# Kernel optimization log

Hardware: AMD Instinct MI355X
Metric: run time of the kernel (lower is better)

Reference implementation:

```python
import jax, jax.numpy as jnp
import numpy as np

N0, E0 = 50000, 200000
N1 = E0 // 2          # 100000 path nodes (pairs of graph0 edges)
E1 = 400000
ATOM_F, BOND_F, IN_F, H = 128, 128, 64, 2


def _egat(src, dst, n_nodes, nfeats, efeats, W_ni, W_nj, W_fij, W_node, b_node, attn, bias, out_n, out_e):
    # edge feature: f_ni[src] + f_nj[dst] + fc_fij(efeats) + bias
    f = (nfeats @ W_ni)[src] + (nfeats @ W_nj)[dst] + efeats @ W_fij + bias
    f = jax.nn.leaky_relu(f).reshape(-1, H, out_e)          # [E, H, out_e]
    e = jnp.sum(f * attn, axis=-1)                          # [E, H] attention logits
    # edge softmax over incoming edges of each dst node
    emax = jax.ops.segment_max(e, dst, num_segments=n_nodes)
    ee = jnp.exp(e - emax[dst])
    a = ee / jax.ops.segment_sum(ee, dst, num_segments=n_nodes)[dst]   # [E, H]
    h = (nfeats @ W_node + b_node).reshape(-1, H, out_n)    # [N, H, out_n]
    h_out = jax.ops.segment_sum(h[src] * a[..., None], dst, num_segments=n_nodes)
    return h_out, f


def setup_inputs() -> dict:
    key = jax.random.key(0)
    it = iter(jax.random.split(key, 64))
    def nrm(shape, s=0.1):
        return jax.random.normal(next(it), shape, jnp.float32) * s
    inp = {
        'node_feats': nrm((N0, ATOM_F), 1.0),
        'edge_feats': nrm((E0, BOND_F), 1.0),
        'node_path': nrm((N1, BOND_F), 1.0),
        'edge_path': nrm((E1, IN_F), 1.0),
    }
    def egat_params(pre, in_n, in_e, out_n, out_e):
        inp[pre + '_ni'] = nrm((in_n, out_e * H))
        inp[pre + '_nj'] = nrm((in_n, out_e * H))
        inp[pre + '_fij'] = nrm((in_e, out_e * H))
        inp[pre + '_node'] = nrm((in_n, out_n * H))
        inp[pre + '_bnode'] = nrm((out_n * H,))
        inp[pre + '_attn'] = nrm((1, H, out_e))
        inp[pre + '_bias'] = nrm((out_e * H,))
    egat_params('L1', ATOM_F, BOND_F, ATOM_F, BOND_F)
    egat_params('L2a', BOND_F, IN_F, BOND_F, IN_F)
    egat_params('L2b', BOND_F, IN_F, BOND_F, IN_F)
    egat_params('L3', ATOM_F, BOND_F, ATOM_F, BOND_F)
    inp['lin1_W'] = nrm((2 * BOND_F, BOND_F))
    inp['lin1_b'] = nrm((BOND_F,))
    # graphs: arange prefix on dst guarantees in-degree >= 1 for every node
    inp['src0'] = jax.random.randint(next(it), (E0,), 0, N0)
    inp['dst0'] = jnp.concatenate([jnp.arange(N0), jax.random.randint(next(it), (E0 - N0,), 0, N0)])
    inp['src1'] = jax.random.randint(next(it), (E1,), 0, N1)
    inp['dst1'] = jnp.concatenate([jnp.arange(N1), jax.random.randint(next(it), (E1 - N1,), 0, N1)])
    return inp


def reference(node_feats, edge_feats, node_path, edge_path,
              L1_ni, L1_nj, L1_fij, L1_node, L1_bnode, L1_attn, L1_bias,
              L2a_ni, L2a_nj, L2a_fij, L2a_node, L2a_bnode, L2a_attn, L2a_bias,
              L2b_ni, L2b_nj, L2b_fij, L2b_node, L2b_bnode, L2b_attn, L2b_bias,
              L3_ni, L3_nj, L3_fij, L3_node, L3_bnode, L3_attn, L3_bias,
              lin1_W, lin1_b, src0, dst0, src1, dst1):
    ini_y3 = node_path
    # ---- stage 1: EGAT on atom graph ----
    h, f = _egat(src0, dst0, N0, node_feats, edge_feats,
                 L1_ni, L1_nj, L1_fij, L1_node, L1_bnode, L1_attn, L1_bias, ATOM_F, BOND_F)
    nf = h.sum(axis=1)            # [N0, ATOM_F]
    ef = f.sum(axis=1)            # [E0, BOND_F]
    # ---- edge-pair -> path-node lift ----
    x11 = jnp.concatenate([ef[0::2], ef[1::2]], axis=1)     # [N1, 2*BOND_F]
    node_path = x11 @ lin1_W + lin1_b + ini_y3              # [N1, BOND_F]
    # ---- stage 2: EGAT layers on path graph ----
    for p in ((L2a_ni, L2a_nj, L2a_fij, L2a_node, L2a_bnode, L2a_attn, L2a_bias),
              (L2b_ni, L2b_nj, L2b_fij, L2b_node, L2b_bnode, L2b_attn, L2b_bias)):
        h, f = _egat(src1, dst1, N1, node_path, edge_path, *p, BOND_F, IN_F)
        node_path = h.sum(axis=1)  # [N1, BOND_F]
        edge_path = f.sum(axis=1)  # [E1, IN_F]
    # ---- path-node -> edge feats for atom graph (each row repeated twice) ----
    ef2 = jnp.repeat(node_path, 2, axis=0)                  # [E0, BOND_F]
    # ---- stage 3: EGAT on atom graph again ----
    h, f = _egat(src0, dst0, N0, nf, ef2,
                 L3_ni, L3_nj, L3_fij, L3_node, L3_bnode, L3_attn, L3_bias, ATOM_F, BOND_F)
    nf = h.sum(axis=1)
    ef2 = f.sum(axis=1)
    return (nf, ef2, node_path, edge_path)
```

## Files before the change

### kernel.cpp

```cpp
#include <hip/hip_runtime.h>

#define CN0 50000
#define CE0 200000
#define CN1 100000
#define CE1 400000

typedef __attribute__((ext_vector_type(8))) _Float16 half8;
typedef __attribute__((ext_vector_type(4))) _Float16 half4;
typedef __attribute__((ext_vector_type(4))) float floatx4;

__global__ void fill_k(float* __restrict__ p, float v, int n) {
    int i = blockIdx.x * 256 + threadIdx.x;
    if (i < n) p[i] = v;
}

struct WtDesc { const float* W; _Float16* T; int KM; int mshift; int K; };
struct WtArgs { WtDesc d[17]; };

__global__ __launch_bounds__(256) void wcvt_k(WtArgs a) {
    WtDesc w = a.d[blockIdx.y];
    const int M1 = (1 << w.mshift) - 1;
    for (int i = blockIdx.x * 256 + threadIdx.x; i < w.KM; i += 256 * gridDim.x) {
        int k = i >> w.mshift, m = i & M1;
        w.T[(long)m * w.K + k] = (_Float16)w.W[i];
    }
}

__global__ void hist2_k(const int* __restrict__ dst0, const int* __restrict__ dst1,
                        int* __restrict__ deg0, int* __restrict__ deg1) {
    int i = blockIdx.x * 256 + threadIdx.x;
    if (i < CE0) atomicAdd(&deg0[dst0[i]], 1);
    if (i < CE1) atomicAdd(&deg1[dst1[i]], 1);
}

__global__ __launch_bounds__(256) void scanA_k(const int* __restrict__ deg, int N,
                                               int* __restrict__ off, int* __restrict__ bsum) {
    __shared__ int s[256];
    int t = threadIdx.x, i = blockIdx.x * 256 + t;
    int v = (i < N) ? deg[i] : 0;
    s[t] = v; __syncthreads();
    #pragma unroll
    for (int d = 1; d < 256; d <<= 1) {
        int x = (t >= d) ? s[t - d] : 0;
        __syncthreads(); s[t] += x; __syncthreads();
    }
    if (i < N) off[i] = s[t] - v;
    if (t == 255) bsum[blockIdx.x] = s[255];
}

__global__ __launch_bounds__(256) void scanB_k(int* __restrict__ bsum0, int nb0,
                                               int* __restrict__ bsum1, int nb1) {
    int* bs = blockIdx.x ? bsum1 : bsum0;
    int nb  = blockIdx.x ? nb1 : nb0;
    __shared__ int s[256];
    __shared__ int tot, carry;
    int t = threadIdx.x;
    if (t == 0) carry = 0;
    __syncthreads();
    for (int base = 0; base < nb; base += 256) {
        int i = base + t;
        int v = (i < nb) ? bs[i] : 0;
        s[t] = v; __syncthreads();
        #pragma unroll
        for (int d = 1; d < 256; d <<= 1) {
            int x = (t >= d) ? s[t - d] : 0;
            __syncthreads(); s[t] += x; __syncthreads();
        }
        if (i < nb) bs[i] = s[t] - v + carry;
        if (t == 255) tot = s[255];
        __syncthreads();
        if (t == 0) carry += tot;
        __syncthreads();
    }
}

__global__ void scanC_k(int* __restrict__ off, const int* __restrict__ bsum, int N, int E) {
    int i = blockIdx.x * 256 + threadIdx.x;
    if (i < N) off[i] += bsum[i >> 8];
    if (i == 0) off[N] = E;
}

__global__ void csrfill2_k(const int* __restrict__ dst0, const int* __restrict__ off0,
                           int* __restrict__ cur0, int* __restrict__ eidx0,
                           const int* __restrict__ dst1, const int* __restrict__ off1,
                           int* __restrict__ cur1, int* __restrict__ eidx1) {
    int i = blockIdx.x * 256 + threadIdx.x;
    if (i < CE0) {
        int d = dst0[i];
        int s = atomicAdd(&cur0[d], 1);
        eidx0[off0[d] + s] = i;
    }
    if (i < CE1) {
        int d = dst1[i];
        int s = atomicAdd(&cur1[d], 1);
        eidx1[off1[d] + s] = i;
    }
}

__global__ __launch_bounds__(256) void gemm_k(
        const float* __restrict__ X, const _Float16* __restrict__ Wt,
        const float* __restrict__ bias, const float* __restrict__ add,
        float* __restrict__ Y, int N, int K, int M) {
    __shared__ _Float16 As[128 * 64];
    char* asb = (char*)As;
    const int tid = threadIdx.x;
    const int lane = tid & 63;
    const int wid = tid >> 6;
    const int wr = wid >> 1, wc = wid & 1;
    const int bm = blockIdx.y * 128;
    const int bn = blockIdx.x * 128;
    const int l15 = lane & 15, lk = lane >> 4;

    floatx4 acc[4][4] = {};

    for (int k0 = 0; k0 < K; k0 += 64) {
        #pragma unroll
        for (int i = 0; i < 8; ++i) {
            int f = tid + i * 256;
            int r = f >> 4, kq = f & 15;
            int gr = bm + r;
            float4 v = make_float4(0.f, 0.f, 0.f, 0.f);
            if (gr < N) v = *(const float4*)&X[(long)gr * K + k0 + kq * 4];
            half4 hv = { (_Float16)v.x, (_Float16)v.y, (_Float16)v.z, (_Float16)v.w };
            int byte = (r * 128 + kq * 8) ^ ((r & 7) << 4);
            *(half4*)(asb + byte) = hv;
        }
        half8 bf[2][4];
        #pragma unroll
        for (int kk = 0; kk < 2; ++kk)
            #pragma unroll
            for (int ct = 0; ct < 4; ++ct) {
                int col = bn + wc * 64 + ct * 16 + l15;
                bf[kk][ct] = *(const half8*)&Wt[(long)col * K + k0 + kk * 32 + lk * 8];
            }
        __syncthreads();
        #pragma unroll
        for (int kk = 0; kk < 2; ++kk) {
            half8 af[4];
            #pragma unroll
            for (int rt = 0; rt < 4; ++rt) {
                int row = wr * 64 + rt * 16 + l15;
                int byte = (row * 128 + (kk * 32 + lk * 8) * 2) ^ ((row & 7) << 4);
                af[rt] = *(const half8*)(asb + byte);
            }
            #pragma unroll
            for (int rt = 0; rt < 4; ++rt)
                #pragma unroll
                for (int ct = 0; ct < 4; ++ct)
                    acc[rt][ct] = __builtin_amdgcn_mfma_f32_16x16x32_f16(
                        af[rt], bf[kk][ct], acc[rt][ct], 0, 0, 0);
        }
        __syncthreads();
    }
    #pragma unroll
    for (int ct = 0; ct < 4; ++ct) {
        int col = bn + wc * 64 + ct * 16 + l15;
        float bv = bias ? bias[col] : 0.f;
        #pragma unroll
        for (int rt = 0; rt < 4; ++rt) {
            #pragma unroll
            for (int r = 0; r < 4; ++r) {
                int row = bm + wr * 64 + rt * 16 + lk * 4 + r;
                if (row < N) {
                    float v = acc[rt][ct][r] + bv;
                    long off = (long)row * M + col;
                    if (add) v += add[off];
                    Y[off] = v;
                }
            }
        }
    }
}

__global__ __launch_bounds__(256) void edge_k(
        const float* __restrict__ FNi, const float* __restrict__ FNj,
        const float* __restrict__ FEb, const float* __restrict__ attn,
        const int* __restrict__ src, const int* __restrict__ dst,
        int E, int out_e, int fe_shift,
        float* __restrict__ ef_out, float* __restrict__ logits) {
    int e = blockIdx.x * 4 + (threadIdx.x >> 6);
    int lane = threadIdx.x & 63;
    if (e >= E) return;
    int s = src[e], d = dst[e];
    long fi = (long)s * (2 * out_e);
    long fj = (long)d * (2 * out_e);
    long fe = (long)(e >> fe_shift) * (2 * out_e);
    float l0 = 0.f, l1 = 0.f;
    for (int c = lane; c < out_e; c += 64) {
        float f0 = FNi[fi + c] + FNj[fj + c] + FEb[fe + c];
        f0 = f0 > 0.f ? f0 : 0.01f * f0;
        float f1 = FNi[fi + out_e + c] + FNj[fj + out_e + c] + FEb[fe + out_e + c];
        f1 = f1 > 0.f ? f1 : 0.01f * f1;
        l0 += f0 * attn[c];
        l1 += f1 * attn[out_e + c];
        ef_out[(long)e * out_e + c] = f0 + f1;
    }
    #pragma unroll
    for (int off = 32; off > 0; off >>= 1) {
        l0 += __shfl_down(l0, off);
        l1 += __shfl_down(l1, off);
    }
    if (lane == 0) { logits[2 * e] = l0; logits[2 * e + 1] = l1; }
}

__global__ __launch_bounds__(256) void aggregate_k(
        const float* __restrict__ Hn, const float* __restrict__ logits,
        const int* __restrict__ off, const int* __restrict__ eidx,
        const int* __restrict__ src, int N, float* __restrict__ out) {
    int n = blockIdx.x * 4 + (threadIdx.x >> 6);
    int lane = threadIdx.x & 63;
    if (n >= N) return;
    int i0 = off[n], i1 = off[n + 1];
    float m0 = -3.0e38f, m1 = -3.0e38f;
    for (int i = i0; i < i1; ++i) {
        int e = eidx[i];
        m0 = fmaxf(m0, logits[2 * e]);
        m1 = fmaxf(m1, logits[2 * e + 1]);
    }
    float s0 = 0.f, s1 = 0.f;
    for (int i = i0; i < i1; ++i) {
        int e = eidx[i];
        s0 += __expf(logits[2 * e]     - m0);
        s1 += __expf(logits[2 * e + 1] - m1);
    }
    float r0 = 1.f / s0, r1 = 1.f / s1;
    float acc0 = 0.f, acc1 = 0.f;
    for (int i = i0; i < i1; ++i) {
        int e = eidx[i];
        float w0 = __expf(logits[2 * e]     - m0) * r0;
        float w1 = __expf(logits[2 * e + 1] - m1) * r1;
        const float* h = Hn + (long)src[e] * 256;
        acc0 += w0 * h[lane]      + w1 * h[128 + lane];
        acc1 += w0 * h[64 + lane] + w1 * h[192 + lane];
    }
    float* o = out + (long)n * 128;
    o[lane]      = acc0;
    o[64 + lane] = acc1;
}

extern "C" void kernel_launch(void* const* d_in, const int* in_sizes, int n_in,
                              void* d_out, int out_size, void* d_ws, size_t ws_size,
                              hipStream_t stream) {
    const float* node_feats   = (const float*)d_in[0];
    const float* edge_feats   = (const float*)d_in[1];
    const float* node_path_in = (const float*)d_in[2];
    const float* edge_path_in = (const float*)d_in[3];
    const float* lin1_b = (const float*)d_in[33];
    const int* src0 = (const int*)d_in[34];
    const int* dst0 = (const int*)d_in[35];
    const int* src1 = (const int*)d_in[36];
    const int* dst1 = (const int*)d_in[37];

    float* out  = (float*)d_out;
    float* seg0 = out;
    float* seg1 = out + 6400000;
    float* seg2 = out + 32000000;
    float* seg3 = out + 44800000;

    float* ws     = (float*)d_ws;
    float* FNi    = ws;
    float* FNj    = FNi + 12800000;
    float* Hn     = FNj + 12800000;
    float* FE     = Hn  + 25600000;
    float* EF     = FE  + 51200000;
    float* np2    = EF  + 25600000;
    float* logits = np2 + 12800000;
    _Float16* WT  = (_Float16*)(logits + 800000);
    int* ib    = (int*)(WT + 442368);
    int* off0  = ib;
    int* eidx0 = off0 + 50001;
    int* off1  = eidx0 + 200000;
    int* eidx1 = off1 + 100001;
    int* deg0  = eidx1 + 400000;
    int* cur0  = deg0 + 50000;
    int* deg1  = cur0 + 50000;
    int* cur1  = deg1 + 100000;
    int* bsum0 = cur1 + 100000;
    int* bsum1 = bsum0 + 196;

    const int nb0 = (CN0 + 255) / 256;
    const int nb1 = (CN1 + 255) / 256;

    static const int wi_din[17]  = {4,5,6,7, 11,12,13,14, 18,19,20,21, 25,26,27,28, 32};
    static const int wi_K[17]    = {128,128,128,128, 128,128,64,128, 128,128,64,128, 128,128,128,128, 256};
    static const int wi_M[17]    = {256,256,256,256, 128,128,128,256, 128,128,128,256, 256,256,256,256, 128};
    _Float16* wt[17];
    {
        _Float16* p = WT;
        for (int i = 0; i < 17; ++i) { wt[i] = p; p += (size_t)wi_K[i] * wi_M[i]; }
    }
    {
        WtArgs a;
        for (int i = 0; i < 17; ++i) {
            a.d[i].W = (const float*)d_in[wi_din[i]];
            a.d[i].T = wt[i];
            a.d[i].KM = wi_K[i] * wi_M[i];
            a.d[i].mshift = (wi_M[i] == 256) ? 8 : 7;
            a.d[i].K = wi_K[i];
        }
        wcvt_k<<<dim3(4, 17), 256, 0, stream>>>(a);
    }

    fill_k<<<(300000 + 255) / 256, 256, 0, stream>>>((float*)deg0, 0.f, 300000);
    hist2_k<<<(CE1 + 255) / 256, 256, 0, stream>>>(dst0, dst1, deg0, deg1);
    scanA_k<<<nb0, 256, 0, stream>>>(deg0, CN0, off0, bsum0);
    scanA_k<<<nb1, 256, 0, stream>>>(deg1, CN1, off1, bsum1);
    scanB_k<<<2, 256, 0, stream>>>(bsum0, nb0, bsum1, nb1);
    scanC_k<<<nb0, 256, 0, stream>>>(off0, bsum0, CN0, CE0);
    scanC_k<<<nb1, 256, 0, stream>>>(off1, bsum1, CN1, CE1);
    csrfill2_k<<<(CE1 + 255) / 256, 256, 0, stream>>>(dst0, off0, cur0, eidx0,
                                                      dst1, off1, cur1, eidx1);

    auto gemm = [&](const float* X, const _Float16* Wt, const float* b, const float* add,
                    float* Y, int N, int K, int M) {
        dim3 g(M / 128, (N + 127) / 128);
        gemm_k<<<g, 256, 0, stream>>>(X, Wt, b, add, Y, N, K, M);
    };
    auto egat = [&](const float* nfeats, int N, int in_n,
                    const float* efeats, int fij_rows, int in_e,
                    int out_e, int fe_shift, int base, int wb,
                    const int* src, const int* dst, int E,
                    const int* off, const int* eidx,
                    float* ef_out, float* h_out) {
        const float* bnode = (const float*)d_in[base + 4];
        const float* attn  = (const float*)d_in[base + 5];
        const float* bias  = (const float*)d_in[base + 6];
        gemm(nfeats, wt[wb + 0], nullptr, nullptr, FNi, N, in_n, 2 * out_e);
        gemm(nfeats, wt[wb + 1], nullptr, nullptr, FNj, N, in_n, 2 * out_e);
        gemm(nfeats, wt[wb + 3], bnode,   nullptr, Hn,  N, in_n, 256);
        gemm(efeats, wt[wb + 2], bias,    nullptr, FE,  fij_rows, in_e, 2 * out_e);
        edge_k<<<(E + 3) / 4, 256, 0, stream>>>(FNi, FNj, FE, attn, src, dst,
                                                E, out_e, fe_shift, ef_out, logits);
        aggregate_k<<<(N + 3) / 4, 256, 0, stream>>>(Hn, logits, off, eidx, src, N, h_out);
    };

    egat(node_feats, CN0, 128, edge_feats, CE0, 128, 128, 0, 4, 0,
         src0, dst0, CE0, off0, eidx0, seg1, seg0);

    gemm(seg1, wt[16], lin1_b, node_path_in, seg2, CN1, 256, 128);

    egat(seg2, CN1, 128, edge_path_in, CE1, 64, 64, 0, 11, 4,
         src1, dst1, CE1, off1, eidx1, EF, np2);

    egat(np2, CN1, 128, EF, CE1, 64, 64, 0, 18, 8,
         src1, dst1, CE1, off1, eidx1, seg3, seg2);

    egat(seg0, CN0, 128, seg2, CN1, 128, 128, 1, 25, 12,
         src0, dst0, CE0, off0, eidx0, seg1, seg0);
}
```

Before: 2.656 ms.

## Store CSR-ordered logits and sources; fuse softmax-sum with aggregation loop

The CSR build now stores each edge's source id in CSR order and records each edge's CSR slot. edge_k scatters its two logits to that slot as a float2, so aggregate_k reads logits and sources contiguously instead of chasing eidx indirections. The denominator and the weighted sum are merged into one pass, with normalization applied at the end, and feature loads and stores are vectorized as float2. This adds a scattered write in edge_k and extra workspace for pos arrays, but removes two indirect gathers per edge and one loop over the neighborhood in aggregation.

```diff
diff --git a/kernel.cpp b/kernel.cpp
--- a/kernel.cpp
+++ b/kernel.cpp
@@ -80,20 +80,24 @@
     if (i == 0) off[N] = E;
 }
 
-__global__ void csrfill2_k(const int* __restrict__ dst0, const int* __restrict__ off0,
-                           int* __restrict__ cur0, int* __restrict__ eidx0,
-                           const int* __restrict__ dst1, const int* __restrict__ off1,
-                           int* __restrict__ cur1, int* __restrict__ eidx1) {
+__global__ void csrfill2_k(const int* __restrict__ src0, const int* __restrict__ dst0,
+                           const int* __restrict__ off0, int* __restrict__ cur0,
+                           int* __restrict__ csrc0, int* __restrict__ pos0,
+                           const int* __restrict__ src1, const int* __restrict__ dst1,
+                           const int* __restrict__ off1, int* __restrict__ cur1,
+                           int* __restrict__ csrc1, int* __restrict__ pos1) {
     int i = blockIdx.x * 256 + threadIdx.x;
     if (i < CE0) {
         int d = dst0[i];
-        int s = atomicAdd(&cur0[d], 1);
-        eidx0[off0[d] + s] = i;
+        int slot = off0[d] + atomicAdd(&cur0[d], 1);
+        csrc0[slot] = src0[i];
+        pos0[i] = slot;
     }
     if (i < CE1) {
         int d = dst1[i];
-        int s = atomicAdd(&cur1[d], 1);
-        eidx1[off1[d] + s] = i;
+        int slot = off1[d] + atomicAdd(&cur1[d], 1);
+        csrc1[slot] = src1[i];
+        pos1[i] = slot;
     }
 }
 
@@ -176,8 +180,9 @@
         const float* __restrict__ FNi, const float* __restrict__ FNj,
         const float* __restrict__ FEb, const float* __restrict__ attn,
         const int* __restrict__ src, const int* __restrict__ dst,
+        const int* __restrict__ pos,
         int E, int out_e, int fe_shift,
-        float* __restrict__ ef_out, float* __restrict__ logits) {
+        float* __restrict__ ef_out, float* __restrict__ clog) {
     int e = blockIdx.x * 4 + (threadIdx.x >> 6);
     int lane = threadIdx.x & 63;
     if (e >= E) return;
@@ -200,42 +205,45 @@
         l0 += __shfl_down(l0, off);
         l1 += __shfl_down(l1, off);
     }
-    if (lane == 0) { logits[2 * e] = l0; logits[2 * e + 1] = l1; }
+    if (lane == 0) {
+        int p = pos[e];
+        float2 lv = { l0, l1 };
+        *(float2*)&clog[2 * p] = lv;
+    }
 }
 
 __global__ __launch_bounds__(256) void aggregate_k(
-        const float* __restrict__ Hn, const float* __restrict__ logits,
-        const int* __restrict__ off, const int* __restrict__ eidx,
-        const int* __restrict__ src, int N, float* __restrict__ out) {
+        const float* __restrict__ Hn, const float* __restrict__ clog,
+        const int* __restrict__ off, const int* __restrict__ csrc,
+        int N, float* __restrict__ out) {
     int n = blockIdx.x * 4 + (threadIdx.x >> 6);
     int lane = threadIdx.x & 63;
     if (n >= N) return;
     int i0 = off[n], i1 = off[n + 1];
     float m0 = -3.0e38f, m1 = -3.0e38f;
     for (int i = i0; i < i1; ++i) {
-        int e = eidx[i];
-        m0 = fmaxf(m0, logits[2 * e]);
-        m1 = fmaxf(m1, logits[2 * e + 1]);
+        float2 l = *(const float2*)&clog[2 * i];
+        m0 = fmaxf(m0, l.x);
+        m1 = fmaxf(m1, l.y);
     }
     float s0 = 0.f, s1 = 0.f;
+    float2 accA = make_float2(0.f, 0.f), accB = make_float2(0.f, 0.f);
     for (int i = i0; i < i1; ++i) {
-        int e = eidx[i];
-        s0 += __expf(logits[2 * e]     - m0);
-        s1 += __expf(logits[2 * e + 1] - m1);
+        float2 l = *(const float2*)&clog[2 * i];
+        float w0 = __expf(l.x - m0);
+        float w1 = __expf(l.y - m1);
+        s0 += w0; s1 += w1;
+        const float* h = Hn + (long)csrc[i] * 256;
+        float2 h0 = *(const float2*)&h[2 * lane];
+        float2 h1 = *(const float2*)&h[128 + 2 * lane];
+        accA.x += w0 * h0.x; accA.y += w0 * h0.y;
+        accB.x += w1 * h1.x; accB.y += w1 * h1.y;
     }
     float r0 = 1.f / s0, r1 = 1.f / s1;
-    float acc0 = 0.f, acc1 = 0.f;
-    for (int i = i0; i < i1; ++i) {
-        int e = eidx[i];
-        float w0 = __expf(logits[2 * e]     - m0) * r0;
-        float w1 = __expf(logits[2 * e + 1] - m1) * r1;
-        const float* h = Hn + (long)src[e] * 256;
-        acc0 += w0 * h[lane]      + w1 * h[128 + lane];
-        acc1 += w0 * h[64 + lane] + w1 * h[192 + lane];
-    }
-    float* o = out + (long)n * 128;
-    o[lane]      = acc0;
-    o[64 + lane] = acc1;
+    float2 o;
+    o.x = accA.x * r0 + accB.x * r1;
+    o.y = accA.y * r0 + accB.y * r1;
+    *(float2*)&out[(long)n * 128 + 2 * lane] = o;
 }
 
 extern "C" void kernel_launch(void* const* d_in, const int* in_sizes, int n_in,
@@ -268,10 +276,12 @@
     _Float16* WT  = (_Float16*)(logits + 800000);
     int* ib    = (int*)(WT + 442368);
     int* off0  = ib;
-    int* eidx0 = off0 + 50001;
-    int* off1  = eidx0 + 200000;
-    int* eidx1 = off1 + 100001;
-    int* deg0  = eidx1 + 400000;
+    int* csrc0 = off0 + 50001;
+    int* off1  = csrc0 + 200000;
+    int* csrc1 = off1 + 100001;
+    int* pos0  = csrc1 + 400000;
+    int* pos1  = pos0 + 200000;
+    int* deg0  = pos1 + 400000;
     int* cur0  = deg0 + 50000;
     int* deg1  = cur0 + 50000;
     int* cur1  = deg1 + 100000;
@@ -308,8 +318,8 @@
     scanB_k<<<2, 256, 0, stream>>>(bsum0, nb0, bsum1, nb1);
     scanC_k<<<nb0, 256, 0, stream>>>(off0, bsum0, CN0, CE0);
     scanC_k<<<nb1, 256, 0, stream>>>(off1, bsum1, CN1, CE1);
-    csrfill2_k<<<(CE1 + 255) / 256, 256, 0, stream>>>(dst0, off0, cur0, eidx0,
-                                                      dst1, off1, cur1, eidx1);
+    csrfill2_k<<<(CE1 + 255) / 256, 256, 0, stream>>>(src0, dst0, off0, cur0, csrc0, pos0,
+                                                      src1, dst1, off1, cur1, csrc1, pos1);
 
     auto gemm = [&](const float* X, const _Float16* Wt, const float* b, const float* add,
                     float* Y, int N, int K, int M) {
@@ -320,7 +330,7 @@
                     const float* efeats, int fij_rows, int in_e,
                     int out_e, int fe_shift, int base, int wb,
                     const int* src, const int* dst, int E,
-                    const int* off, const int* eidx,
+                    const int* off, const int* csrc, const int* pos,
                     float* ef_out, float* h_out) {
         const float* bnode = (const float*)d_in[base + 4];
         const float* attn  = (const float*)d_in[base + 5];
@@ -329,22 +339,22 @@
         gemm(nfeats, wt[wb + 1], nullptr, nullptr, FNj, N, in_n, 2 * out_e);
         gemm(nfeats, wt[wb + 3], bnode,   nullptr, Hn,  N, in_n, 256);
         gemm(efeats, wt[wb + 2], bias,    nullptr, FE,  fij_rows, in_e, 2 * out_e);
-        edge_k<<<(E + 3) / 4, 256, 0, stream>>>(FNi, FNj, FE, attn, src, dst,
+        edge_k<<<(E + 3) / 4, 256, 0, stream>>>(FNi, FNj, FE, attn, src, dst, pos,
                                                 E, out_e, fe_shift, ef_out, logits);
-        aggregate_k<<<(N + 3) / 4, 256, 0, stream>>>(Hn, logits, off, eidx, src, N, h_out);
+        aggregate_k<<<(N + 3) / 4, 256, 0, stream>>>(Hn, logits, off, csrc, N, h_out);
     };
 
     egat(node_feats, CN0, 128, edge_feats, CE0, 128, 128, 0, 4, 0,
-         src0, dst0, CE0, off0, eidx0, seg1, seg0);
+         src0, dst0, CE0, off0, csrc0, pos0, seg1, seg0);
 
     gemm(seg1, wt[16], lin1_b, node_path_in, seg2, CN1, 256, 128);
 
     egat(seg2, CN1, 128, edge_path_in, CE1, 64, 64, 0, 11, 4,
-         src1, dst1, CE1, off1, eidx1, EF, np2);
+         src1, dst1, CE1, off1, csrc1, pos1, EF, np2);
 
     egat(np2, CN1, 128, EF, CE1, 64, 64, 0, 18, 8,
-         src1, dst1, CE1, off1, eidx1, seg3, seg2);
+         src1, dst1, CE1, off1, csrc1, pos1, seg3, seg2);
 
     egat(seg0, CN0, 128, seg2, CN1, 128, 128, 1, 25, 12,
-         src0, dst0, CE0, off0, eidx0, seg1, seg0);
-}
+         src0, dst0, CE0, off0, csrc0, pos0, seg1, seg0);
+}
```

After: 2.483 ms. 6.5% less time.
